# Optimization experiments

Hardware: AMD Instinct MI355X
Metric: run time of the kernel (lower is better)

The kernel has to match this reference:

```python
import jax, jax.numpy as jnp
import numpy as np

B, S, D = 2, 2048, 1024
H, HD = 16, 64          # num_heads, head_dim (D == H*HD)
FF = 4 * D
EPS = 1e-5

def _xavier(key, shape):
    fan_out, fan_in = shape
    lim = np.sqrt(6.0 / (fan_in + fan_out))
    return jax.random.uniform(key, shape, jnp.float32, -lim, lim)

def setup_inputs() -> dict:
    key = jax.random.key(0)
    ks = jax.random.split(key, 8)
    return {
        "x": jax.random.normal(ks[0], (B, S, D), jnp.float32),
        "g1": jnp.ones((D,), jnp.float32), "b1": jnp.zeros((D,), jnp.float32),
        "Wqkv": _xavier(ks[1], (3 * D, D)), "bqkv": jnp.zeros((3 * D,), jnp.float32),
        "Wo": _xavier(ks[2], (D, D)), "bo": jnp.zeros((D,), jnp.float32),
        "g2": jnp.ones((D,), jnp.float32), "b2": jnp.zeros((D,), jnp.float32),
        "W1": _xavier(ks[3], (FF, D)), "b1m": jnp.zeros((FF,), jnp.float32),
        "W2": _xavier(ks[4], (D, FF)), "b2m": jnp.zeros((D,), jnp.float32),
    }

def _ln(x, g, b):
    m = jnp.mean(x, axis=-1, keepdims=True)
    v = jnp.var(x, axis=-1, keepdims=True)
    return (x - m) * jax.lax.rsqrt(v + EPS) * g + b

def reference(x, g1, b1, Wqkv, bqkv, Wo, bo, g2, b2, W1, b1m, W2, b2m):
    # --- pre-norm attention ---
    h = _ln(x, g1, b1)
    qkv = h @ Wqkv.T + bqkv                                  # [B,S,3D]
    qkv = qkv.reshape(B, S, H, 3 * HD).transpose(0, 2, 1, 3)  # [B,H,S,3hd]
    q, k, v = jnp.split(qkv, 3, axis=-1)                      # each [B,H,S,hd]
    scores = jnp.einsum('bhqd,bhkd->bhqk', q, k) / np.sqrt(HD).astype(np.float32)
    att = jax.nn.softmax(scores, axis=-1)                     # [B,H,S,S]
    vals = jnp.einsum('bhqk,bhkd->bhqd', att, v)
    vals = vals.transpose(0, 2, 1, 3).reshape(B, S, D)
    x = x + (vals @ Wo.T + bo)
    # --- pre-norm MLP (dropouts inactive in eval) ---
    h = _ln(x, g2, b2)
    h = jax.nn.gelu(h @ W1.T + b1m, approximate=False)
    x = x + (h @ W2.T + b2m)
    return x
```

## Files before the change

### kernel.cpp

```cpp
#include <hip/hip_runtime.h>
#include <math.h>

#define BB 2
#define SS 2048
#define DD 1024
#define HH 16
#define FFDIM 4096
#define NROWS 4096

typedef short bf16x8 __attribute__((ext_vector_type(8)));
typedef float f32x4 __attribute__((ext_vector_type(4)));

__device__ __forceinline__ unsigned short f2bf(float f) {
    unsigned u = __float_as_uint(f);
    u += 0x7fffu + ((u >> 16) & 1u);
    return (unsigned short)(u >> 16);
}

typedef __attribute__((address_space(1))) void gvoid;
typedef __attribute__((address_space(3))) void lvoid;
__device__ __forceinline__ void glds16(const void* g, void* l) {
    __builtin_amdgcn_global_load_lds((gvoid*)g, (lvoid*)l, 16, 0, 0);
}

__global__ __launch_bounds__(256) void ln_kernel(const float* __restrict__ x,
                                                 const float* __restrict__ g,
                                                 const float* __restrict__ b,
                                                 unsigned short* __restrict__ out) {
    int row = blockIdx.x;
    const float* xr = x + (size_t)row * DD;
    unsigned short* orow = out + (size_t)row * DD;
    int t = threadIdx.x;
    float4 v = ((const float4*)xr)[t];
    float s  = v.x + v.y + v.z + v.w;
    float s2 = v.x*v.x + v.y*v.y + v.z*v.z + v.w*v.w;
    #pragma unroll
    for (int off = 32; off > 0; off >>= 1) {
        s  += __shfl_down(s,  off);
        s2 += __shfl_down(s2, off);
    }
    __shared__ float red1[4], red2[4];
    int wid = t >> 6, lane = t & 63;
    if (lane == 0) { red1[wid] = s; red2[wid] = s2; }
    __syncthreads();
    if (t == 0) {
        float a = 0.f, a2 = 0.f;
        #pragma unroll
        for (int i = 0; i < 4; ++i) { a += red1[i]; a2 += red2[i]; }
        red1[0] = a; red2[0] = a2;
    }
    __syncthreads();
    float mean = red1[0] * (1.0f / DD);
    float var  = red2[0] * (1.0f / DD) - mean * mean;
    float rs = rsqrtf(var + 1e-5f);
    float4 gv = ((const float4*)g)[t];
    float4 bv = ((const float4*)b)[t];
    ushort4 o;
    o.x = f2bf((v.x - mean) * rs * gv.x + bv.x);
    o.y = f2bf((v.y - mean) * rs * gv.y + bv.y);
    o.z = f2bf((v.z - mean) * rs * gv.z + bv.z);
    o.w = f2bf((v.w - mean) * rs * gv.w + bv.w);
    ((ushort4*)orow)[t] = o;
}

__global__ __launch_bounds__(256) void cast4(const float* __restrict__ a, unsigned short* __restrict__ oa,
                                             const float* __restrict__ b, unsigned short* __restrict__ ob,
                                             const float* __restrict__ c, unsigned short* __restrict__ oc,
                                             const float* __restrict__ d, unsigned short* __restrict__ od) {
    int i = blockIdx.x * 256 + threadIdx.x;
    const float* src; unsigned short* dst; int off;
    if (i < 786432)       { src = a; dst = oa; off = i; }
    else if (i < 1048576) { src = b; dst = ob; off = i - 786432; }
    else if (i < 2097152) { src = c; dst = oc; off = i - 1048576; }
    else                  { src = d; dst = od; off = i - 2097152; }
    float4 v = ((const float4*)src)[off];
    ushort4 o;
    o.x = f2bf(v.x); o.y = f2bf(v.y); o.z = f2bf(v.z); o.w = f2bf(v.w);
    ((ushort4*)dst)[off] = o;
}

template<int ACT, int RES, int OUTBF, int TN, int VT>
__global__ __launch_bounds__(256, 3) void gemm_nt_mfma(
    const unsigned short* __restrict__ A,
    const unsigned short* __restrict__ W,
    const float* __restrict__ bias,
    const float* __restrict__ res,
    void* __restrict__ Cout,
    unsigned short* __restrict__ Vtg,
    int M, int N, int K)
{
    constexpr int MI = (TN == 128) ? 4 : 2;
    constexpr int WR = TN / 4;
    __shared__ unsigned short As[128 * 64];
    __shared__ unsigned short Ws[TN * 64];
    int tid = threadIdx.x;
    int lane = tid & 63;
    int w = tid >> 6;
    int rowbase = (TN == 128) ? ((w >> 1) * 64) : (w * 32);
    int colbase = (TN == 128) ? ((w & 1) * 64) : 0;
    int bm = blockIdx.y * 128, bn = blockIdx.x * TN;
    int col16 = lane & 15, quad = lane >> 4;

    f32x4 acc[MI][4] = {};

    int lrow = lane >> 3;
    int sw = (lane & 7) ^ lrow;
    const unsigned short* Ag = A + (size_t)(bm + w * 32 + lrow) * K + sw * 8;
    const unsigned short* Wg = W + (size_t)(bn + w * WR + lrow) * K + sw * 8;

    for (int k0 = 0; k0 < K; k0 += 64) {
        if (k0) __syncthreads();
        #pragma unroll
        for (int it = 0; it < 4; ++it)
            glds16(Ag + (size_t)(8 * it) * K + k0, &As[(w * 32 + 8 * it) * 64]);
        #pragma unroll
        for (int it = 0; it < WR / 8; ++it)
            glds16(Wg + (size_t)(8 * it) * K + k0, &Ws[(w * WR + 8 * it) * 64]);
        __syncthreads();
        #pragma unroll
        for (int c = 0; c < 2; ++c) {
            bf16x8 af[MI], bfr[4];
            #pragma unroll
            for (int i = 0; i < MI; ++i) {
                int m = rowbase + i * 16 + col16;
                af[i] = *(const bf16x8*)&As[m * 64 + (((c * 4 + quad) ^ (m & 7)) * 8)];
            }
            #pragma unroll
            for (int j = 0; j < 4; ++j) {
                int n = colbase + j * 16 + col16;
                bfr[j] = *(const bf16x8*)&Ws[n * 64 + (((c * 4 + quad) ^ (n & 7)) * 8)];
            }
            #pragma unroll
            for (int i = 0; i < MI; ++i)
                #pragma unroll
                for (int j = 0; j < 4; ++j)
                    acc[i][j] = __builtin_amdgcn_mfma_f32_16x16x32_bf16(af[i], bfr[j], acc[i][j], 0, 0, 0);
        }
    }

    #pragma unroll
    for (int i = 0; i < MI; ++i) {
        #pragma unroll
        for (int j = 0; j < 4; ++j) {
            int nnb = bn + colbase + j * 16;
            int nn = nnb + col16;
            float bv = bias[nn];
            float vv[4];
            #pragma unroll
            for (int r = 0; r < 4; ++r) {
                float v = acc[i][j][r] + bv;
                if (ACT) v = 0.5f * v * (1.0f + erff(v * 0.70710678118654752f));
                vv[r] = v;
            }
            int mm0 = bm + rowbase + i * 16 + quad * 4;
            if (VT && ((nnb >> 6) % 3) == 2) {
                int hh = nnb / 192;
                int d = nn - hh * 192 - 128;
                int bb = mm0 >> 11, sr = mm0 & 2047;
                ushort4 pkv;
                pkv.x = f2bf(vv[0]); pkv.y = f2bf(vv[1]);
                pkv.z = f2bf(vv[2]); pkv.w = f2bf(vv[3]);
                *(ushort4*)&Vtg[((size_t)((bb * HH + hh) * 64 + d)) * (size_t)SS + sr] = pkv;
            } else {
                #pragma unroll
                for (int r = 0; r < 4; ++r) {
                    int mm = mm0 + r;
                    float v = vv[r];
                    if (RES) v += res[(size_t)mm * N + nn];
                    if (OUTBF) ((unsigned short*)Cout)[(size_t)mm * N + nn] = f2bf(v);
                    else       ((float*)Cout)[(size_t)mm * N + nn] = v;
                }
            }
        }
    }
}

__global__ __launch_bounds__(256, 4) void attn_mfma(
    const unsigned short* __restrict__ qkv,
    const unsigned short* __restrict__ Vtg,
    unsigned short* __restrict__ outb)
{
    __shared__ unsigned short Ks[128 * 64];
    __shared__ unsigned short VtL[64 * 128];
    int tid = threadIdx.x;
    int lane = tid & 63;
    int wv = tid >> 6;
    int qt = blockIdx.x, h = blockIdx.y, b = blockIdx.z;
    int col16 = lane & 15, quad = lane >> 4;

    const unsigned short* qbase = qkv + (size_t)(b * SS) * 3072;
    const unsigned short* Kg = qbase + h * 192 + 64;
    const unsigned short* Vg = Vtg + ((size_t)(b * HH + h) * 64) * (size_t)SS;

    int qrow = qt * 64 + wv * 16 + col16;
    bf16x8 qf[2];
    qf[0] = *(const bf16x8*)&qbase[(size_t)qrow * 3072 + h * 192 + quad * 8];
    qf[1] = *(const bf16x8*)&qbase[(size_t)qrow * 3072 + h * 192 + 32 + quad * 8];

    f32x4 o[4] = {};
    float lsum = 0.f;
    const float C = 0.18033688011112042f;

    for (int s0 = 0; s0 < SS; s0 += 128) {
        if (s0) __syncthreads();
        #pragma unroll
        for (int p = 0; p < 4; ++p) {
            int ci = (p * 4 + wv) * 64 + lane;
            int k = ci >> 3, sk = ci & 7, qk = sk ^ (k & 7);
            glds16(Kg + (size_t)(s0 + k) * 3072 + qk * 8, &Ks[ci * 8]);
            int dv = ci >> 4, sv = ci & 15, qv = sv ^ (dv & 7);
            glds16(Vg + (size_t)dv * SS + s0 + qv * 8, &VtL[ci * 8]);
        }
        __syncthreads();

        f32x4 st[8];
        #pragma unroll
        for (int t = 0; t < 8; ++t) {
            f32x4 z = {};
            st[t] = z;
            int key = t * 16 + col16;
            #pragma unroll
            for (int c = 0; c < 2; ++c) {
                bf16x8 kf = *(const bf16x8*)&Ks[key * 64 + (((c * 4 + quad) ^ (key & 7)) * 8)];
                st[t] = __builtin_amdgcn_mfma_f32_16x16x32_bf16(kf, qf[c], st[t], 0, 0, 0);
            }
        }

        unsigned lo[8], hi[8];
        float psum = 0.f;
        #pragma unroll
        for (int t = 0; t < 8; ++t) {
            float p0 = exp2f(st[t][0] * C);
            float p1 = exp2f(st[t][1] * C);
            float p2 = exp2f(st[t][2] * C);
            float p3 = exp2f(st[t][3] * C);
            psum += (p0 + p1) + (p2 + p3);
            lo[t] = __builtin_amdgcn_perm(__float_as_uint(p1), __float_as_uint(p0), 0x07060302u);
            hi[t] = __builtin_amdgcn_perm(__float_as_uint(p3), __float_as_uint(p2), 0x07060302u);
        }
        psum += __shfl_xor(psum, 16);
        psum += __shfl_xor(psum, 32);
        lsum += psum;

        #pragma unroll
        for (int kc = 0; kc < 4; ++kc) {
            int sa = ((quad & 1) << 5) + col16;
            unsigned a0 = __shfl((int)lo[2*kc],   sa);
            unsigned b0 = __shfl((int)lo[2*kc+1], sa);
            unsigned a1 = __shfl((int)hi[2*kc],   sa);
            unsigned b1 = __shfl((int)hi[2*kc+1], sa);
            unsigned a2 = __shfl((int)lo[2*kc],   sa + 16);
            unsigned b2 = __shfl((int)lo[2*kc+1], sa + 16);
            unsigned a3 = __shfl((int)hi[2*kc],   sa + 16);
            unsigned b3 = __shfl((int)hi[2*kc+1], sa + 16);
            bool gs = quad >= 2;
            uint4 pk;
            pk.x = gs ? b0 : a0;
            pk.y = gs ? b1 : a1;
            pk.z = gs ? b2 : a2;
            pk.w = gs ? b3 : a3;
            bf16x8 pf = *(bf16x8*)&pk;
            #pragma unroll
            for (int nt = 0; nt < 4; ++nt) {
                int d = nt * 16 + col16;
                bf16x8 vf = *(const bf16x8*)&VtL[d * 128 + (((kc * 4 + quad) ^ (d & 7)) * 8)];
                o[nt] = __builtin_amdgcn_mfma_f32_16x16x32_bf16(pf, vf, o[nt], 0, 0, 0);
            }
        }
    }

    float linv = 1.0f / lsum;
    float linv_r[4];
    #pragma unroll
    for (int r = 0; r < 4; ++r) linv_r[r] = __shfl(linv, quad * 4 + r);

    int orow0 = b * SS + qt * 64 + wv * 16;
    #pragma unroll
    for (int r = 0; r < 4; ++r) {
        int mm = orow0 + quad * 4 + r;
        #pragma unroll
        for (int nt = 0; nt < 4; ++nt)
            outb[(size_t)mm * DD + h * 64 + nt * 16 + col16] = f2bf(o[nt][r] * linv_r[r]);
    }
}

extern "C" void kernel_launch(void* const* d_in, const int* in_sizes, int n_in,
                              void* d_out, int out_size, void* d_ws, size_t ws_size,
                              hipStream_t stream) {
    const float* x    = (const float*)d_in[0];
    const float* g1   = (const float*)d_in[1];
    const float* b1   = (const float*)d_in[2];
    const float* Wqkv = (const float*)d_in[3];
    const float* bqkv = (const float*)d_in[4];
    const float* Wo   = (const float*)d_in[5];
    const float* bo   = (const float*)d_in[6];
    const float* g2   = (const float*)d_in[7];
    const float* b2   = (const float*)d_in[8];
    const float* W1   = (const float*)d_in[9];
    const float* b1m  = (const float*)d_in[10];
    const float* W2   = (const float*)d_in[11];
    const float* b2m  = (const float*)d_in[12];
    float* out = (float*)d_out;

    char* wsb = (char*)d_ws;
    unsigned short* Wq_b  = (unsigned short*)(wsb);
    unsigned short* Wo_b  = (unsigned short*)(wsb + 6291456);
    unsigned short* W1_b  = (unsigned short*)(wsb + 8388608);
    unsigned short* W2_b  = (unsigned short*)(wsb + 16777216);
    unsigned short* hb    = (unsigned short*)(wsb + 25165824);
    unsigned short* qkvb  = (unsigned short*)(wsb + 33554432);
    unsigned short* attnb = (unsigned short*)(wsb + 58720256);
    float*          x1    = (float*)(wsb + 67108864);
    unsigned short* ffb   = (unsigned short*)(wsb + 83886080);
    unsigned short* Vtg   = (unsigned short*)(wsb + 83886080);

    cast4<<<12288, 256, 0, stream>>>(Wqkv, Wq_b, Wo, Wo_b, W1, W1_b, W2, W2_b);

    ln_kernel<<<NROWS, 256, 0, stream>>>(x, g1, b1, hb);
    gemm_nt_mfma<0,0,1,128,1><<<dim3(24, 32), 256, 0, stream>>>(hb, Wq_b, bqkv, nullptr, qkvb,
                                                                Vtg, NROWS, 3 * DD, DD);
    attn_mfma<<<dim3(SS / 64, HH, BB), 256, 0, stream>>>(qkvb, Vtg, attnb);
    gemm_nt_mfma<0,1,0,64,0><<<dim3(16, 32), 256, 0, stream>>>(attnb, Wo_b, bo, x, x1,
                                                               nullptr, NROWS, DD, DD);
    ln_kernel<<<NROWS, 256, 0, stream>>>(x1, g2, b2, hb);
    gemm_nt_mfma<1,0,1,128,0><<<dim3(32, 32), 256, 0, stream>>>(hb, W1_b, b1m, nullptr, ffb,
                                                                nullptr, NROWS, FFDIM, DD);
    gemm_nt_mfma<0,1,0,64,0><<<dim3(16, 32), 256, 0, stream>>>(ffb, W2_b, b2m, x1, out,
                                                               nullptr, NROWS, DD, FFDIM);
}
```

Before: 366.2 us.

## Stage GEMM epilogues through LDS, use tanh-GELU, and simplify attention P packing

The W1 GEMM epilogue now writes bf16 results into a swizzled LDS tile and stores them with coalesced 16-byte writes. The QKV GEMM now transposes V in LDS before writing it out. Exact erf GELU is replaced by a tanh-style sigmoid approximation built from fast exp2 and rcp. In attention, the softmax scale is folded into Q, hardware exp2 and rcp intrinsics are used, and the shuffle-based repacking of P is dropped because V's key order is permuted to match. These cut scattered global stores, transcendental cost and cross-lane shuffles, at the price of extra LDS traffic and syncs, plus some approximation error in GELU and in Q rounding.

```diff
diff --git a/kernel.cpp b/kernel.cpp
--- a/kernel.cpp
+++ b/kernel.cpp
@@ -21,6 +21,10 @@
 typedef __attribute__((address_space(3))) void lvoid;
 __device__ __forceinline__ void glds16(const void* g, void* l) {
     __builtin_amdgcn_global_load_lds((gvoid*)g, (lvoid*)l, 16, 0, 0);
+}
+
+__device__ __forceinline__ int vkey(int kloc) {
+    return (kloc & ~31) + ((kloc & 12) << 1) + ((kloc & 16) >> 2);
 }
 
 __global__ __launch_bounds__(256) void ln_kernel(const float* __restrict__ x,
@@ -79,7 +83,7 @@
     ((ushort4*)dst)[off] = o;
 }
 
-template<int ACT, int RES, int OUTBF, int TN, int VT>
+template<int ACT, int RES, int OUTBF, int TN, int VT, int CS>
 __global__ __launch_bounds__(256, 3) void gemm_nt_mfma(
     const unsigned short* __restrict__ A,
     const unsigned short* __restrict__ W,
@@ -91,8 +95,9 @@
 {
     constexpr int MI = (TN == 128) ? 4 : 2;
     constexpr int WR = TN / 4;
-    __shared__ unsigned short As[128 * 64];
-    __shared__ unsigned short Ws[TN * 64];
+    __shared__ unsigned short SMEM[128 * 64 + TN * 64];
+    unsigned short* As = SMEM;
+    unsigned short* Ws = SMEM + 128 * 64;
     int tid = threadIdx.x;
     int lane = tid & 63;
     int w = tid >> 6;
@@ -138,29 +143,70 @@
         }
     }
 
+    if constexpr (CS) {
+        __syncthreads();
+        #pragma unroll
+        for (int i = 0; i < MI; ++i) {
+            #pragma unroll
+            for (int j = 0; j < 4; ++j) {
+                int nl = colbase + j * 16 + col16;
+                float bv = bias[bn + nl];
+                int c = nl >> 4;
+                #pragma unroll
+                for (int r = 0; r < 4; ++r) {
+                    int ml = rowbase + i * 16 + quad * 4 + r;
+                    float v = acc[i][j][r] + bv;
+                    if (ACT) {
+                        float z = v * (1.595769122f + 0.071354816f * v * v);
+                        float e = __builtin_amdgcn_exp2f(-z * 1.442695041f);
+                        v = v * __builtin_amdgcn_rcpf(1.0f + e);
+                    }
+                    SMEM[ml * 128 + ((c ^ ((ml >> 2) & 7)) << 4) + (nl & 15)] = f2bf(v);
+                }
+            }
+        }
+        __syncthreads();
+        #pragma unroll
+        for (int p = 0; p < 8; ++p) {
+            int cid = tid + p * 256;
+            int row = cid >> 4, cc = cid & 15;
+            int cs2 = cc >> 1;
+            bf16x8 vv = *(bf16x8*)&SMEM[row * 128 + ((cs2 ^ ((row >> 2) & 7)) << 4) + (cc & 1) * 8];
+            *(bf16x8*)&((unsigned short*)Cout)[(size_t)(bm + row) * N + bn + cc * 8] = vv;
+        }
+        return;
+    }
+
+    bool wave_v = VT && ((((bn + colbase) >> 6) % 3) == 2);
+    if constexpr (VT) __syncthreads();
+
     #pragma unroll
     for (int i = 0; i < MI; ++i) {
         #pragma unroll
         for (int j = 0; j < 4; ++j) {
-            int nnb = bn + colbase + j * 16;
-            int nn = nnb + col16;
+            int nn = bn + colbase + j * 16 + col16;
             float bv = bias[nn];
             float vv[4];
             #pragma unroll
             for (int r = 0; r < 4; ++r) {
                 float v = acc[i][j][r] + bv;
-                if (ACT) v = 0.5f * v * (1.0f + erff(v * 0.70710678118654752f));
+                if (ACT) {
+                    float z = v * (1.595769122f + 0.071354816f * v * v);
+                    float e = __builtin_amdgcn_exp2f(-z * 1.442695041f);
+                    v = v * __builtin_amdgcn_rcpf(1.0f + e);
+                }
                 vv[r] = v;
             }
             int mm0 = bm + rowbase + i * 16 + quad * 4;
-            if (VT && ((nnb >> 6) % 3) == 2) {
-                int hh = nnb / 192;
-                int d = nn - hh * 192 - 128;
-                int bb = mm0 >> 11, sr = mm0 & 2047;
-                ushort4 pkv;
-                pkv.x = f2bf(vv[0]); pkv.y = f2bf(vv[1]);
-                pkv.z = f2bf(vv[2]); pkv.w = f2bf(vv[3]);
-                *(ushort4*)&Vtg[((size_t)((bb * HH + hh) * 64 + d)) * (size_t)SS + sr] = pkv;
+            if (VT && wave_v) {
+                int d = j * 16 + col16;
+                int kloc = rowbase + i * 16 + quad * 4;
+                int vl = vkey(kloc);
+                int ch = vl >> 3;
+                ushort4 pk;
+                pk.x = f2bf(vv[0]); pk.y = f2bf(vv[1]);
+                pk.z = f2bf(vv[2]); pk.w = f2bf(vv[3]);
+                *(ushort4*)&SMEM[d * 128 + ((ch ^ (d & 7)) << 3) + (vl & 7)] = pk;
             } else {
                 #pragma unroll
                 for (int r = 0; r < 4; ++r) {
@@ -170,6 +216,24 @@
                     if (OUTBF) ((unsigned short*)Cout)[(size_t)mm * N + nn] = f2bf(v);
                     else       ((float*)Cout)[(size_t)mm * N + nn] = v;
                 }
+            }
+        }
+    }
+
+    if constexpr (VT) {
+        __syncthreads();
+        bool g0v = ((bn >> 6) % 3) == 2;
+        bool g1v = (((bn + 64) >> 6) % 3) == 2;
+        if (g0v || g1v) {
+            int vcb = g0v ? 0 : 64;
+            int hh = (bn + vcb) / 192;
+            int bb = bm >> 11, sr = bm & 2047;
+            #pragma unroll
+            for (int p = 0; p < 4; ++p) {
+                int cid = tid + p * 256;
+                int d = cid >> 4, ch = cid & 15;
+                bf16x8 vv2 = *(bf16x8*)&SMEM[d * 128 + ((ch ^ (d & 7)) << 3)];
+                *(bf16x8*)&Vtg[((size_t)((bb * HH + hh) * 64 + d)) * (size_t)SS + sr + ch * 8] = vv2;
             }
         }
     }
@@ -192,14 +256,21 @@
     const unsigned short* Kg = qbase + h * 192 + 64;
     const unsigned short* Vg = Vtg + ((size_t)(b * HH + h) * 64) * (size_t)SS;
 
+    const float C = 0.18033688011112042f;
     int qrow = qt * 64 + wv * 16 + col16;
     bf16x8 qf[2];
     qf[0] = *(const bf16x8*)&qbase[(size_t)qrow * 3072 + h * 192 + quad * 8];
     qf[1] = *(const bf16x8*)&qbase[(size_t)qrow * 3072 + h * 192 + 32 + quad * 8];
+    #pragma unroll
+    for (int c = 0; c < 2; ++c)
+        #pragma unroll
+        for (int i = 0; i < 8; ++i) {
+            float f = __uint_as_float(((unsigned)(unsigned short)qf[c][i]) << 16) * C;
+            qf[c][i] = (short)f2bf(f);
+        }
 
     f32x4 o[4] = {};
     float lsum = 0.f;
-    const float C = 0.18033688011112042f;
 
     for (int s0 = 0; s0 < SS; s0 += 128) {
         if (s0) __syncthreads();
@@ -230,10 +301,10 @@
         float psum = 0.f;
         #pragma unroll
         for (int t = 0; t < 8; ++t) {
-            float p0 = exp2f(st[t][0] * C);
-            float p1 = exp2f(st[t][1] * C);
-            float p2 = exp2f(st[t][2] * C);
-            float p3 = exp2f(st[t][3] * C);
+            float p0 = __builtin_amdgcn_exp2f(st[t][0]);
+            float p1 = __builtin_amdgcn_exp2f(st[t][1]);
+            float p2 = __builtin_amdgcn_exp2f(st[t][2]);
+            float p3 = __builtin_amdgcn_exp2f(st[t][3]);
             psum += (p0 + p1) + (p2 + p3);
             lo[t] = __builtin_amdgcn_perm(__float_as_uint(p1), __float_as_uint(p0), 0x07060302u);
             hi[t] = __builtin_amdgcn_perm(__float_as_uint(p3), __float_as_uint(p2), 0x07060302u);
@@ -244,21 +315,9 @@
 
         #pragma unroll
         for (int kc = 0; kc < 4; ++kc) {
-            int sa = ((quad & 1) << 5) + col16;
-            unsigned a0 = __shfl((int)lo[2*kc],   sa);
-            unsigned b0 = __shfl((int)lo[2*kc+1], sa);
-            unsigned a1 = __shfl((int)hi[2*kc],   sa);
-            unsigned b1 = __shfl((int)hi[2*kc+1], sa);
-            unsigned a2 = __shfl((int)lo[2*kc],   sa + 16);
-            unsigned b2 = __shfl((int)lo[2*kc+1], sa + 16);
-            unsigned a3 = __shfl((int)hi[2*kc],   sa + 16);
-            unsigned b3 = __shfl((int)hi[2*kc+1], sa + 16);
-            bool gs = quad >= 2;
             uint4 pk;
-            pk.x = gs ? b0 : a0;
-            pk.y = gs ? b1 : a1;
-            pk.z = gs ? b2 : a2;
-            pk.w = gs ? b3 : a3;
+            pk.x = lo[2 * kc]; pk.y = hi[2 * kc];
+            pk.z = lo[2 * kc + 1]; pk.w = hi[2 * kc + 1];
             bf16x8 pf = *(bf16x8*)&pk;
             #pragma unroll
             for (int nt = 0; nt < 4; ++nt) {
@@ -269,7 +328,7 @@
         }
     }
 
-    float linv = 1.0f / lsum;
+    float linv = __builtin_amdgcn_rcpf(lsum);
     float linv_r[4];
     #pragma unroll
     for (int r = 0; r < 4; ++r) linv_r[r] = __shfl(linv, quad * 4 + r);
@@ -317,14 +376,14 @@
     cast4<<<12288, 256, 0, stream>>>(Wqkv, Wq_b, Wo, Wo_b, W1, W1_b, W2, W2_b);
 
     ln_kernel<<<NROWS, 256, 0, stream>>>(x, g1, b1, hb);
-    gemm_nt_mfma<0,0,1,128,1><<<dim3(24, 32), 256, 0, stream>>>(hb, Wq_b, bqkv, nullptr, qkvb,
-                                                                Vtg, NROWS, 3 * DD, DD);
+    gemm_nt_mfma<0,0,1,128,1,0><<<dim3(24, 32), 256, 0, stream>>>(hb, Wq_b, bqkv, nullptr, qkvb,
+                                                                  Vtg, NROWS, 3 * DD, DD);
     attn_mfma<<<dim3(SS / 64, HH, BB), 256, 0, stream>>>(qkvb, Vtg, attnb);
-    gemm_nt_mfma<0,1,0,64,0><<<dim3(16, 32), 256, 0, stream>>>(attnb, Wo_b, bo, x, x1,
-                                                               nullptr, NROWS, DD, DD);
+    gemm_nt_mfma<0,1,0,64,0,0><<<dim3(16, 32), 256, 0, stream>>>(attnb, Wo_b, bo, x, x1,
+                                                                 nullptr, NROWS, DD, DD);
     ln_kernel<<<NROWS, 256, 0, stream>>>(x1, g2, b2, hb);
-    gemm_nt_mfma<1,0,1,128,0><<<dim3(32, 32), 256, 0, stream>>>(hb, W1_b, b1m, nullptr, ffb,
-                                                                nullptr, NROWS, FFDIM, DD);
-    gemm_nt_mfma<0,1,0,64,0><<<dim3(16, 32), 256, 0, stream>>>(ffb, W2_b, b2m, x1, out,
-                                                               nullptr, NROWS, DD, FFDIM);
-}
+    gemm_nt_mfma<1,0,1,128,0,1><<<dim3(32, 32), 256, 0, stream>>>(hb, W1_b, b1m, nullptr, ffb,
+                                                                  nullptr, NROWS, FFDIM, DD);
+    gemm_nt_mfma<0,1,0,64,0,0><<<dim3(16, 32), 256, 0, stream>>>(ffb, W2_b, b2m, x1, out,
+                                                                 nullptr, NROWS, DD, FFDIM);
+}
```

Result: faster. 330.7 us (-9.7%).
